# Kernel optimization log

Measured on AMD Instinct MI355X. Metric: run time of the kernel, lower is better.

The kernel has to match this reference:

```python
import jax, jax.numpy as jnp
import numpy as np

B, LQ, LK, D = 4, 256, 512, 256


def setup_inputs() -> dict:
    key = jax.random.key(0)
    k1, k2, k3, k4, k5, k6 = jax.random.split(key, 6)
    return {
        "query": jax.random.normal(k1, (B, LQ, D), dtype=jnp.float32),
        "key": jax.random.normal(k2, (B, LK, D), dtype=jnp.float32),
        "value": jax.random.normal(k3, (B, LK, D), dtype=jnp.float32),
        "W1": jax.random.normal(k4, (D, D), dtype=jnp.float32) * 0.06,
        "W2": jax.random.normal(k5, (D, D), dtype=jnp.float32) * 0.06,
        "v": jax.random.normal(k6, (D,), dtype=jnp.float32) * 0.06,
        "mask": jnp.ones((B, LQ, LK), dtype=jnp.int32),
    }


def reference(query, key, value, W1, W2, v, mask):
    # Linear layers are applied to the broadcast tensors in the original, but
    # they distribute over the add: W1(key) and W2(query) computed once each.
    hid_dim = query.shape[-1]
    scale = jnp.sqrt(jnp.asarray(hid_dim, dtype=query.dtype))
    W1_key = jnp.einsum("bkd,ed->bke", key, W1)     # [B, Lk, D]
    W2_query = jnp.einsum("bqd,ed->bqe", query, W2)  # [B, Lq, D]
    # tanh is nonlinear -> the [B, Lq, Lk, D] broadcast-add intermediate is
    # required by the math (this is the kernel-fusion opportunity).
    energy = jnp.tanh(W1_key[:, None, :, :] + W2_query[:, :, None, :])
    scores = jnp.einsum("bqkd,d->bqk", energy, v) / scale  # [B, Lq, Lk]
    scores = jnp.where(mask == 0, jnp.asarray(-1e10, scores.dtype), scores)
    attention = jax.nn.softmax(scores, axis=-1)
    context = jnp.einsum("bqk,bkd->bqd", attention, value)  # [B, Lq, D]
    return (context, attention)
```

## Files before the change

### kernel.cpp

```cpp
#include <hip/hip_runtime.h>
#include <math.h>

#define DD  256
#define LKK 512
#define LQQ 256
#define BB  4

constexpr float TWO_LOG2E = 2.8853900817779268f;
constexpr float LOG2E     = 1.4426950408889634f;

__device__ __forceinline__ float fast_rcp(float x)  { return __builtin_amdgcn_rcpf(x); }
__device__ __forceinline__ float fast_exp2(float x) { return __builtin_amdgcn_exp2f(x); }

__device__ __forceinline__ const float* uni(const float* p) {
  unsigned long long a = (unsigned long long)p;
  unsigned lo = __builtin_amdgcn_readfirstlane((unsigned)a);
  unsigned hi = __builtin_amdgcn_readfirstlane((unsigned)(a >> 32));
  return (const float*)(((unsigned long long)hi << 32) | lo);
}

#define COMP(v,u) ((u)==0?(v).x:(u)==1?(v).y:(u)==2?(v).z:(v).w)

__global__ __launch_bounds__(256) void gemm_expk2(const float* __restrict__ key,
                                                  const float* __restrict__ query,
                                                  const float* __restrict__ W1,
                                                  const float* __restrict__ W2,
                                                  float* __restrict__ EaT,
                                                  float* __restrict__ Eb) {
  __shared__ float Xs[32][36];
  __shared__ float Ws[32][68];
  const int tid = threadIdx.x;
  const bool isK = blockIdx.x < (BB * LKK / 32);
  const float* __restrict__ X = isK ? key : query;
  const float* __restrict__ W = isK ? W1 : W2;
  const int m0 = (isK ? blockIdx.x : blockIdx.x - BB * LKK / 32) * 32;
  const int e0 = blockIdx.y * 64;

  const int r0 = (tid >> 4) << 1;
  const int c0 = (tid & 15) << 2;
  const int xr = tid >> 3, xc = (tid & 7) << 2;
  const int wr = tid >> 2, wc = (tid & 3) << 3;

  float4 xv  = *(const float4*)&X[(m0 + xr) * DD + xc];
  float4 wv0 = *(const float4*)&W[(e0 + wr) * DD + wc];
  float4 wv1 = *(const float4*)&W[(e0 + wr) * DD + wc + 4];

  float acc[2][4] = {};
  for (int k0 = 0; k0 < DD; k0 += 32) {
    __syncthreads();
    Xs[xc + 0][xr] = xv.x; Xs[xc + 1][xr] = xv.y; Xs[xc + 2][xr] = xv.z; Xs[xc + 3][xr] = xv.w;
    Ws[wc + 0][wr] = wv0.x; Ws[wc + 1][wr] = wv0.y; Ws[wc + 2][wr] = wv0.z; Ws[wc + 3][wr] = wv0.w;
    Ws[wc + 4][wr] = wv1.x; Ws[wc + 5][wr] = wv1.y; Ws[wc + 6][wr] = wv1.z; Ws[wc + 7][wr] = wv1.w;
    __syncthreads();
    if (k0 + 32 < DD) {
      xv  = *(const float4*)&X[(m0 + xr) * DD + k0 + 32 + xc];
      wv0 = *(const float4*)&W[(e0 + wr) * DD + k0 + 32 + wc];
      wv1 = *(const float4*)&W[(e0 + wr) * DD + k0 + 32 + wc + 4];
    }
#pragma unroll
    for (int k = 0; k < 32; ++k) {
      const float2 a  = *(const float2*)&Xs[k][r0];
      const float4 bq = *(const float4*)&Ws[k][c0];
      acc[0][0] = fmaf(a.x, bq.x, acc[0][0]); acc[0][1] = fmaf(a.x, bq.y, acc[0][1]);
      acc[0][2] = fmaf(a.x, bq.z, acc[0][2]); acc[0][3] = fmaf(a.x, bq.w, acc[0][3]);
      acc[1][0] = fmaf(a.y, bq.x, acc[1][0]); acc[1][1] = fmaf(a.y, bq.y, acc[1][1]);
      acc[1][2] = fmaf(a.y, bq.z, acc[1][2]); acc[1][3] = fmaf(a.y, bq.w, acc[1][3]);
    }
  }
  if (isK) {
    const int b = m0 >> 9;
    const int kloc = (m0 & 511) + r0;
#pragma unroll
    for (int j = 0; j < 4; ++j) {
      float2 o;
      o.x = fast_exp2(acc[0][j] * TWO_LOG2E);
      o.y = fast_exp2(acc[1][j] * TWO_LOG2E);
      *(float2*)&EaT[b * (DD * LKK) + (e0 + c0 + j) * LKK + kloc] = o;
    }
  } else {
#pragma unroll
    for (int i = 0; i < 2; ++i) {
      float4 o;
      o.x = fast_exp2(acc[i][0] * TWO_LOG2E);
      o.y = fast_exp2(acc[i][1] * TWO_LOG2E);
      o.z = fast_exp2(acc[i][2] * TWO_LOG2E);
      o.w = fast_exp2(acc[i][3] * TWO_LOG2E);
      *(float4*)&Eb[(m0 + r0 + i) * DD + e0 + c0] = o;
    }
  }
}

#define QUAD8(CX, UBL, UBH, ACC) do {                                 \
    const float A_ = fmaf(c0.CX, (UBL).x, 1.f);                       \
    const float B_ = fmaf(c1.CX, (UBL).y, 1.f);                       \
    const float C_ = fmaf(c2.CX, (UBL).z, 1.f);                       \
    const float D_ = fmaf(c3.CX, (UBL).w, 1.f);                       \
    const float E_ = fmaf(c4.CX, (UBH).x, 1.f);                       \
    const float F_ = fmaf(c5.CX, (UBH).y, 1.f);                       \
    const float G_ = fmaf(c6.CX, (UBH).z, 1.f);                       \
    const float H_ = fmaf(c7.CX, (UBH).w, 1.f);                       \
    const float AB_ = A_ * B_, CD_ = C_ * D_;                         \
    const float EF_ = E_ * F_, GH_ = G_ * H_;                         \
    const float t1_ = fmaf(uv0.y, A_, uv0.x * B_);                    \
    const float t2_ = fmaf(uv0.w, C_, uv0.z * D_);                    \
    const float t3_ = fmaf(uv1.y, E_, uv1.x * F_);                    \
    const float t4_ = fmaf(uv1.w, G_, uv1.z * H_);                    \
    const float n1_ = fmaf(t1_, CD_, t2_ * AB_);                      \
    const float n2_ = fmaf(t3_, GH_, t4_ * EF_);                      \
    const float d1_ = AB_ * CD_, d2_ = EF_ * GH_;                     \
    const float nm_ = fmaf(n1_, d2_, n2_ * d1_);                      \
    ACC = fmaf(nm_, fast_rcp(d1_ * d2_), ACC);                        \
  } while (0)

__global__ __launch_bounds__(512) void attn_fused(const float* __restrict__ EaT,
                                                  const float* __restrict__ Eb,
                                                  const float* __restrict__ vvec,
                                                  const float* __restrict__ value,
                                                  const int* __restrict__ mask,
                                                  float* __restrict__ ctx_out,
                                                  float* __restrict__ attn_out) {
  __shared__ float sc[4][LKK];
  __shared__ float buf[16 * LKK];
  __shared__ float svs[4];

  const int tid = threadIdx.x;
  const int bid = blockIdx.x;
  const int b  = bid >> 6;
  const int q0 = (bid & 63) << 2;
  const int dh = tid >> 7;
  const int t  = tid & 127;
  const int k4 = t << 2;
  const int db = dh << 6;

  {
    const float* ebp0 = uni(&Eb[(b * LQQ + q0) * DD + db]);
    const float* ebp1 = uni(&Eb[(b * LQQ + q0 + 1) * DD + db]);
    const float* ebp2 = uni(&Eb[(b * LQQ + q0 + 2) * DD + db]);
    const float* ebp3 = uni(&Eb[(b * LQQ + q0 + 3) * DD + db]);
    const float* vp   = uni(&vvec[db]);

    const float* __restrict__ ea = &EaT[b * (DD * LKK) + db * LKK + k4];
    float4 acc[4] = {};
    float sv = 0.f;

    float4 c0 = *(const float4*)&ea[0 * LKK];
    float4 c1 = *(const float4*)&ea[1 * LKK];
    float4 c2 = *(const float4*)&ea[2 * LKK];
    float4 c3 = *(const float4*)&ea[3 * LKK];
    float4 c4 = *(const float4*)&ea[4 * LKK];
    float4 c5 = *(const float4*)&ea[5 * LKK];
    float4 c6 = *(const float4*)&ea[6 * LKK];
    float4 c7 = *(const float4*)&ea[7 * LKK];
    float4 ubq0l = *(const float4*)&ebp0[0], ubq0h = *(const float4*)&ebp0[4];
    float4 ubq1l = *(const float4*)&ebp1[0], ubq1h = *(const float4*)&ebp1[4];
    float4 ubq2l = *(const float4*)&ebp2[0], ubq2h = *(const float4*)&ebp2[4];
    float4 ubq3l = *(const float4*)&ebp3[0], ubq3h = *(const float4*)&ebp3[4];
    float4 uv0 = *(const float4*)&vp[0], uv1 = *(const float4*)&vp[4];

    for (int d = 0; d < 56; d += 8) {
      const float4 n0 = *(const float4*)&ea[(d +  8) * LKK];
      const float4 n1 = *(const float4*)&ea[(d +  9) * LKK];
      const float4 n2 = *(const float4*)&ea[(d + 10) * LKK];
      const float4 n3 = *(const float4*)&ea[(d + 11) * LKK];
      const float4 n4 = *(const float4*)&ea[(d + 12) * LKK];
      const float4 n5 = *(const float4*)&ea[(d + 13) * LKK];
      const float4 n6 = *(const float4*)&ea[(d + 14) * LKK];
      const float4 n7 = *(const float4*)&ea[(d + 15) * LKK];
      const float4 m0l = *(const float4*)&ebp0[d + 8], m0h = *(const float4*)&ebp0[d + 12];
      const float4 m1l = *(const float4*)&ebp1[d + 8], m1h = *(const float4*)&ebp1[d + 12];
      const float4 m2l = *(const float4*)&ebp2[d + 8], m2h = *(const float4*)&ebp2[d + 12];
      const float4 m3l = *(const float4*)&ebp3[d + 8], m3h = *(const float4*)&ebp3[d + 12];
      const float4 w0 = *(const float4*)&vp[d + 8], w1 = *(const float4*)&vp[d + 12];
      sv += ((uv0.x + uv0.y) + (uv0.z + uv0.w)) + ((uv1.x + uv1.y) + (uv1.z + uv1.w));
      QUAD8(x, ubq0l, ubq0h, acc[0].x); QUAD8(y, ubq0l, ubq0h, acc[0].y);
      QUAD8(z, ubq0l, ubq0h, acc[0].z); QUAD8(w, ubq0l, ubq0h, acc[0].w);
      QUAD8(x, ubq1l, ubq1h, acc[1].x); QUAD8(y, ubq1l, ubq1h, acc[1].y);
      QUAD8(z, ubq1l, ubq1h, acc[1].z); QUAD8(w, ubq1l, ubq1h, acc[1].w);
      QUAD8(x, ubq2l, ubq2h, acc[2].x); QUAD8(y, ubq2l, ubq2h, acc[2].y);
      QUAD8(z, ubq2l, ubq2h, acc[2].z); QUAD8(w, ubq2l, ubq2h, acc[2].w);
      QUAD8(x, ubq3l, ubq3h, acc[3].x); QUAD8(y, ubq3l, ubq3h, acc[3].y);
      QUAD8(z, ubq3l, ubq3h, acc[3].z); QUAD8(w, ubq3l, ubq3h, acc[3].w);
      c0 = n0; c1 = n1; c2 = n2; c3 = n3; c4 = n4; c5 = n5; c6 = n6; c7 = n7;
      ubq0l = m0l; ubq0h = m0h; ubq1l = m1l; ubq1h = m1h;
      ubq2l = m2l; ubq2h = m2h; ubq3l = m3l; ubq3h = m3h;
      uv0 = w0; uv1 = w1;
    }
    sv += ((uv0.x + uv0.y) + (uv0.z + uv0.w)) + ((uv1.x + uv1.y) + (uv1.z + uv1.w));
    QUAD8(x, ubq0l, ubq0h, acc[0].x); QUAD8(y, ubq0l, ubq0h, acc[0].y);
    QUAD8(z, ubq0l, ubq0h, acc[0].z); QUAD8(w, ubq0l, ubq0h, acc[0].w);
    QUAD8(x, ubq1l, ubq1h, acc[1].x); QUAD8(y, ubq1l, ubq1h, acc[1].y);
    QUAD8(z, ubq1l, ubq1h, acc[1].z); QUAD8(w, ubq1l, ubq1h, acc[1].w);
    QUAD8(x, ubq2l, ubq2h, acc[2].x); QUAD8(y, ubq2l, ubq2h, acc[2].y);
    QUAD8(z, ubq2l, ubq2h, acc[2].z); QUAD8(w, ubq2l, ubq2h, acc[2].w);
    QUAD8(x, ubq3l, ubq3h, acc[3].x); QUAD8(y, ubq3l, ubq3h, acc[3].y);
    QUAD8(z, ubq3l, ubq3h, acc[3].z); QUAD8(w, ubq3l, ubq3h, acc[3].w);

#pragma unroll
    for (int q = 0; q < 4; ++q)
      *(float4*)&buf[(dh * 4 + q) * LKK + k4] = acc[q];
    if (t == 0) svs[dh] = sv;
  }
  __syncthreads();

  {
    const int q  = tid >> 7;
    const int kc = (tid & 127) << 2;
    const float Sv = (svs[0] + svs[1]) + (svs[2] + svs[3]);
    const float4 p0 = *(const float4*)&buf[(0 * 4 + q) * LKK + kc];
    const float4 p1 = *(const float4*)&buf[(1 * 4 + q) * LKK + kc];
    const float4 p2 = *(const float4*)&buf[(2 * 4 + q) * LKK + kc];
    const float4 p3 = *(const float4*)&buf[(3 * 4 + q) * LKK + kc];
    const float inv_scale = 0.0625f;
    float4 s;
    s.x = (Sv - 2.f * ((p0.x + p1.x) + (p2.x + p3.x))) * inv_scale;
    s.y = (Sv - 2.f * ((p0.y + p1.y) + (p2.y + p3.y))) * inv_scale;
    s.z = (Sv - 2.f * ((p0.z + p1.z) + (p2.z + p3.z))) * inv_scale;
    s.w = (Sv - 2.f * ((p0.w + p1.w) + (p2.w + p3.w))) * inv_scale;
    const int4 mq = *(const int4*)&mask[(b * LQQ + q0 + q) * LKK + kc];
    if (mq.x == 0) s.x = -1e10f;
    if (mq.y == 0) s.y = -1e10f;
    if (mq.z == 0) s.z = -1e10f;
    if (mq.w == 0) s.w = -1e10f;
    *(float4*)&sc[q][kc] = s;
  }
  __syncthreads();

  {
    const int w = tid >> 6, lane = tid & 63;
    if (w < 4) {
      float e_[8];
      float mx = -3.4e38f;
#pragma unroll
      for (int i = 0; i < 8; ++i) { e_[i] = sc[w][(i << 6) + lane]; mx = fmaxf(mx, e_[i]); }
#pragma unroll
      for (int off = 32; off; off >>= 1) mx = fmaxf(mx, __shfl_xor(mx, off));
      float sum = 0.f;
#pragma unroll
      for (int i = 0; i < 8; ++i) { e_[i] = fast_exp2((e_[i] - mx) * LOG2E); sum += e_[i]; }
#pragma unroll
      for (int off = 32; off; off >>= 1) sum += __shfl_xor(sum, off);
      const float inv = fast_rcp(sum);
      const int arow = (b * LQQ + q0 + w) * LKK;
#pragma unroll
      for (int i = 0; i < 8; ++i) {
        const float p = e_[i] * inv;
        attn_out[arow + (i << 6) + lane] = p;
        sc[w][(i << 6) + lane] = p;
      }
    }
  }
  __syncthreads();

  {
    const int kh = tid >> 6, dv = (tid & 63) << 2;
    const int kb = kh << 6;
    float4 c[4] = {};
    const float* __restrict__ vb = &value[(b * LKK + kb) * DD + dv];
    for (int s = 0; s < 64; s += 4) {
      const float4 p0v = *(const float4*)&sc[0][kb + s];
      const float4 p1v = *(const float4*)&sc[1][kb + s];
      const float4 p2v = *(const float4*)&sc[2][kb + s];
      const float4 p3v = *(const float4*)&sc[3][kb + s];
#pragma unroll
      for (int u = 0; u < 4; ++u) {
        const float4 vv = *(const float4*)vb; vb += DD;
        const float a0 = COMP(p0v, u), a1 = COMP(p1v, u);
        const float a2 = COMP(p2v, u), a3 = COMP(p3v, u);
        c[0].x = fmaf(a0, vv.x, c[0].x); c[0].y = fmaf(a0, vv.y, c[0].y);
        c[0].z = fmaf(a0, vv.z, c[0].z); c[0].w = fmaf(a0, vv.w, c[0].w);
        c[1].x = fmaf(a1, vv.x, c[1].x); c[1].y = fmaf(a1, vv.y, c[1].y);
        c[1].z = fmaf(a1, vv.z, c[1].z); c[1].w = fmaf(a1, vv.w, c[1].w);
        c[2].x = fmaf(a2, vv.x, c[2].x); c[2].y = fmaf(a2, vv.y, c[2].y);
        c[2].z = fmaf(a2, vv.z, c[2].z); c[2].w = fmaf(a2, vv.w, c[2].w);
        c[3].x = fmaf(a3, vv.x, c[3].x); c[3].y = fmaf(a3, vv.y, c[3].y);
        c[3].z = fmaf(a3, vv.z, c[3].z); c[3].w = fmaf(a3, vv.w, c[3].w);
      }
    }
    __syncthreads();
#pragma unroll
    for (int q = 0; q < 4; ++q)
      *(float4*)&buf[(kh * 4 + q) * DD + dv] = c[q];
  }
  __syncthreads();

  if (tid < 256) {
    const int qq = tid >> 6, d4 = (tid & 63) << 2;
    float4 s4 = make_float4(0.f, 0.f, 0.f, 0.f);
#pragma unroll
    for (int kh2 = 0; kh2 < 8; ++kh2) {
      const float4 rr = *(const float4*)&buf[(kh2 * 4 + qq) * DD + d4];
      s4.x += rr.x; s4.y += rr.y; s4.z += rr.z; s4.w += rr.w;
    }
    *(float4*)&ctx_out[(b * LQQ + q0 + qq) * DD + d4] = s4;
  }
}

extern "C" void kernel_launch(void* const* d_in, const int* in_sizes, int n_in,
                              void* d_out, int out_size, void* d_ws, size_t ws_size,
                              hipStream_t stream) {
  const float* query = (const float*)d_in[0];
  const float* key   = (const float*)d_in[1];
  const float* value = (const float*)d_in[2];
  const float* W1    = (const float*)d_in[3];
  const float* W2    = (const float*)d_in[4];
  const float* v     = (const float*)d_in[5];
  const int*   mask  = (const int*)d_in[6];

  float* out      = (float*)d_out;
  float* ctx_out  = out;
  float* attn_out = out + BB * LQQ * DD;

  float* EaT = (float*)d_ws;
  float* Eb  = EaT + BB * DD * LKK;

  dim3 g1(BB * LKK / 32 + BB * LQQ / 32, DD / 64);
  gemm_expk2<<<g1, 256, 0, stream>>>(key, query, W1, W2, EaT, Eb);

  attn_fused<<<256, 512, 0, stream>>>(EaT, Eb, v, value, mask, ctx_out, attn_out);
}
```

Before: 40.33 us.

## Split fused attention into scores kernel and softmax-context kernel for more parallelism

Splits the fused attention kernel in two. The first kernel computes masked scores over half the key range per block, with the D reduction split 8 ways (256 to 512 blocks), and writes the raw scores into the attention output buffer. A second kernel reads those scores back, runs the softmax and computes the context, overwriting the buffer with probabilities. This targets low occupancy and a long serial D loop in the score phase, at the cost of an extra launch and a global round trip of the score matrix.

```diff
diff --git a/kernel.cpp b/kernel.cpp
--- a/kernel.cpp
+++ b/kernel.cpp
@@ -112,25 +112,24 @@
     ACC = fmaf(nm_, fast_rcp(d1_ * d2_), ACC);                        \
   } while (0)
 
-__global__ __launch_bounds__(512) void attn_fused(const float* __restrict__ EaT,
-                                                  const float* __restrict__ Eb,
-                                                  const float* __restrict__ vvec,
-                                                  const float* __restrict__ value,
-                                                  const int* __restrict__ mask,
-                                                  float* __restrict__ ctx_out,
-                                                  float* __restrict__ attn_out) {
-  __shared__ float sc[4][LKK];
-  __shared__ float buf[16 * LKK];
-  __shared__ float svs[4];
+__global__ __launch_bounds__(512) void scores_k(const float* __restrict__ EaT,
+                                                const float* __restrict__ Eb,
+                                                const float* __restrict__ vvec,
+                                                const int* __restrict__ mask,
+                                                float* __restrict__ Sws) {
+  __shared__ float buf[8 * 4 * 256];
+  __shared__ float svs[8];
 
   const int tid = threadIdx.x;
   const int bid = blockIdx.x;
-  const int b  = bid >> 6;
-  const int q0 = (bid & 63) << 2;
-  const int dh = tid >> 7;
-  const int t  = tid & 127;
-  const int k4 = t << 2;
-  const int db = dh << 6;
+  const int b  = bid >> 7;
+  const int r  = bid & 127;
+  const int q0 = (r >> 1) << 2;
+  const int kh = (r & 1) << 8;
+  const int dh8 = (tid >> 6);
+  const int kt  = tid & 63;
+  const int k4l = kt << 2;
+  const int db  = dh8 << 5;
 
   {
     const float* ebp0 = uni(&Eb[(b * LQQ + q0) * DD + db]);
@@ -139,7 +138,7 @@
     const float* ebp3 = uni(&Eb[(b * LQQ + q0 + 3) * DD + db]);
     const float* vp   = uni(&vvec[db]);
 
-    const float* __restrict__ ea = &EaT[b * (DD * LKK) + db * LKK + k4];
+    const float* __restrict__ ea = &EaT[b * (DD * LKK) + db * LKK + kh + k4l];
     float4 acc[4] = {};
     float sv = 0.f;
 
@@ -157,7 +156,7 @@
     float4 ubq3l = *(const float4*)&ebp3[0], ubq3h = *(const float4*)&ebp3[4];
     float4 uv0 = *(const float4*)&vp[0], uv1 = *(const float4*)&vp[4];
 
-    for (int d = 0; d < 56; d += 8) {
+    for (int d = 0; d < 24; d += 8) {
       const float4 n0 = *(const float4*)&ea[(d +  8) * LKK];
       const float4 n1 = *(const float4*)&ea[(d +  9) * LKK];
       const float4 n2 = *(const float4*)&ea[(d + 10) * LKK];
@@ -197,31 +196,47 @@
 
 #pragma unroll
     for (int q = 0; q < 4; ++q)
-      *(float4*)&buf[(dh * 4 + q) * LKK + k4] = acc[q];
-    if (t == 0) svs[dh] = sv;
+      *(float4*)&buf[(dh8 * 4 + q) * 256 + k4l] = acc[q];
+    if (kt == 0) svs[dh8] = sv;
   }
   __syncthreads();
 
   {
     const int q  = tid >> 7;
-    const int kc = (tid & 127) << 2;
-    const float Sv = (svs[0] + svs[1]) + (svs[2] + svs[3]);
-    const float4 p0 = *(const float4*)&buf[(0 * 4 + q) * LKK + kc];
-    const float4 p1 = *(const float4*)&buf[(1 * 4 + q) * LKK + kc];
-    const float4 p2 = *(const float4*)&buf[(2 * 4 + q) * LKK + kc];
-    const float4 p3 = *(const float4*)&buf[(3 * 4 + q) * LKK + kc];
+    const int kc = (tid & 127) << 1;
+    const float Sv = ((svs[0] + svs[1]) + (svs[2] + svs[3]))
+                   + ((svs[4] + svs[5]) + (svs[6] + svs[7]));
+    float2 s = make_float2(0.f, 0.f);
+#pragma unroll
+    for (int d = 0; d < 8; ++d) {
+      const float2 p = *(const float2*)&buf[(d * 4 + q) * 256 + kc];
+      s.x += p.x; s.y += p.y;
+    }
     const float inv_scale = 0.0625f;
-    float4 s;
-    s.x = (Sv - 2.f * ((p0.x + p1.x) + (p2.x + p3.x))) * inv_scale;
-    s.y = (Sv - 2.f * ((p0.y + p1.y) + (p2.y + p3.y))) * inv_scale;
-    s.z = (Sv - 2.f * ((p0.z + p1.z) + (p2.z + p3.z))) * inv_scale;
-    s.w = (Sv - 2.f * ((p0.w + p1.w) + (p2.w + p3.w))) * inv_scale;
-    const int4 mq = *(const int4*)&mask[(b * LQQ + q0 + q) * LKK + kc];
+    s.x = (Sv - 2.f * s.x) * inv_scale;
+    s.y = (Sv - 2.f * s.y) * inv_scale;
+    const int row = (b * LQQ + q0 + q) * LKK + kh + kc;
+    const int2 mq = *(const int2*)&mask[row];
     if (mq.x == 0) s.x = -1e10f;
     if (mq.y == 0) s.y = -1e10f;
-    if (mq.z == 0) s.z = -1e10f;
-    if (mq.w == 0) s.w = -1e10f;
-    *(float4*)&sc[q][kc] = s;
+    *(float2*)&Sws[row] = s;
+  }
+}
+
+__global__ __launch_bounds__(512) void smax_ctx(const float* __restrict__ value,
+                                                float* attn_io,
+                                                float* __restrict__ ctx_out) {
+  __shared__ float sc[4][LKK];
+  __shared__ float buf[16 * LKK];
+
+  const int tid = threadIdx.x;
+  const int bid = blockIdx.x;
+  const int b  = bid >> 6;
+  const int q0 = (bid & 63) << 2;
+
+  {
+    const int q = tid >> 7, j4 = (tid & 127) << 2;
+    *(float4*)&sc[q][j4] = *(const float4*)&attn_io[(b * LQQ + q0 + q) * LKK + j4];
   }
   __syncthreads();
 
@@ -244,7 +259,7 @@
 #pragma unroll
       for (int i = 0; i < 8; ++i) {
         const float p = e_[i] * inv;
-        attn_out[arow + (i << 6) + lane] = p;
+        attn_io[arow + (i << 6) + lane] = p;
         sc[w][(i << 6) + lane] = p;
       }
     }
@@ -316,5 +331,7 @@
   dim3 g1(BB * LKK / 32 + BB * LQQ / 32, DD / 64);
   gemm_expk2<<<g1, 256, 0, stream>>>(key, query, W1, W2, EaT, Eb);
 
-  attn_fused<<<256, 512, 0, stream>>>(EaT, Eb, v, value, mask, ctx_out, attn_out);
-}
+  scores_k<<<512, 512, 0, stream>>>(EaT, Eb, v, mask, attn_out);
+
+  smax_ctx<<<256, 512, 0, stream>>>(value, attn_out, ctx_out);
+}
```

Result: slower. 46.41 us (+15.1%).
